# Performance work log

Hardware: AMD Instinct MI355X
Metric: run time of the kernel (lower is better)

## Reference

```python
import jax, jax.numpy as jnp
import numpy as np

VOCAB = 4096
CODE_DIM = 3
DECAY = 0.99
EPS = 1e-05


def setup_inputs() -> dict:
    key = jax.random.key(0)
    k1, k2, k3, k4 = jax.random.split(key, 4)
    feats = jax.random.normal(k1, (4, 8192, CODE_DIM), dtype=jnp.float32)
    embed = jax.random.normal(k2, (VOCAB, CODE_DIM), dtype=jnp.float32)
    ema_cluster_size = jax.random.uniform(k3, (VOCAB,), dtype=jnp.float32)
    ema_weight = jax.random.normal(k4, (VOCAB, CODE_DIM), dtype=jnp.float32)
    return {"feats": feats, "embed": embed,
            "ema_cluster_size": ema_cluster_size, "ema_weight": ema_weight}


def reference(feats, embed, ema_cluster_size, ema_weight):
    B, L, D = feats.shape
    flat = feats.reshape(-1, D)  # (N, D)
    # squared-euclidean distances to all codes: (N, V)
    dist = (jnp.sum(flat * flat, axis=1, keepdims=True)
            - 2.0 * flat @ embed.T
            + jnp.sum(embed * embed, axis=1))
    idx = jnp.argmin(dist, axis=1)  # (N,)
    quant = embed[idx].reshape(B, L, D)

    # EMA codebook update (training mode), done with segment_sum instead of a
    # dense (N, V) one-hot matmul -- same math.
    counts = jax.ops.segment_sum(jnp.ones_like(flat[:, 0]), idx, num_segments=VOCAB)
    sums = jax.ops.segment_sum(flat, idx, num_segments=VOCAB)  # (V, D)
    new_cluster_size = DECAY * ema_cluster_size + (1.0 - DECAY) * counts
    new_ema_weight = DECAY * ema_weight + (1.0 - DECAY) * sums
    n = jnp.sum(new_cluster_size)
    cluster_size = (new_cluster_size + EPS) / (n + VOCAB * EPS) * n
    new_embed = new_ema_weight / cluster_size[:, None]

    # VQ loss with stop-gradients matching torch detach semantics
    loss = (jnp.mean((quant - jax.lax.stop_gradient(feats)) ** 2)
            + 0.25 * jnp.mean((feats - jax.lax.stop_gradient(quant)) ** 2))
    # straight-through estimator
    quant_st = feats + jax.lax.stop_gradient(quant - feats)
    return (quant_st, idx.reshape(B, L), loss,
            new_cluster_size, new_ema_weight, new_embed)
```

## Files before the change

### kernel.cpp

```cpp
#include <hip/hip_runtime.h>
#include <math.h>

#pragma clang fp contract(off)

#define VOCAB 4096
#define NPTS  32768
#define NELEM 98304
#define BLOCK 256
#define NWAVE 4
#define CPW   (VOCAB / NWAVE)
#define PTS_PER_BLOCK 64

__global__ __launch_bounds__(BLOCK) void vq_assign(
    const float* __restrict__ feats, const float* __restrict__ embed,
    float* __restrict__ out_quant, float* __restrict__ out_idx,
    float* __restrict__ counts, float* __restrict__ sums,
    float* __restrict__ sse)
{
  extern __shared__ float smem[];
  float4* codes = (float4*)smem;
  float*  dbuf  = smem;
  int*    ibuf  = (int*)(smem + NWAVE * 64);

  const int tid  = threadIdx.x;
  const int lane = tid & 63;
  const int wv   = tid >> 6;

  for (int c = tid; c < VOCAB; c += BLOCK) {
    float e0 = embed[3 * c + 0];
    float e1 = embed[3 * c + 1];
    float e2 = embed[3 * c + 2];
    float esq = (e0 * e0 + e1 * e1) + e2 * e2;
    codes[c] = make_float4(e0, e1, e2, esq);
  }
  __syncthreads();

  const int p = blockIdx.x * PTS_PER_BLOCK + lane;
  const float x0 = feats[3 * p + 0];
  const float x1 = feats[3 * p + 1];
  const float x2 = feats[3 * p + 2];
  const float xsq = (x0 * x0 + x1 * x1) + x2 * x2;

  float best = INFINITY;
  int   bidx = 0;
  const float4* wc = codes + wv * CPW;
  const int cbase = wv * CPW;

  #pragma unroll 16
  for (int k = 0; k < CPW; ++k) {
    float4 e = wc[k];
    float dot = fmaf(x2, e.z, fmaf(x1, e.y, x0 * e.x));
    float d = (xsq - 2.0f * dot) + e.w;
    if (d < best) { best = d; bidx = cbase + k; }
  }

  __syncthreads();
  dbuf[wv * 64 + lane] = best;
  ibuf[wv * 64 + lane] = bidx;
  __syncthreads();

  if (wv == 0) {
    #pragma unroll
    for (int w = 1; w < NWAVE; ++w) {
      float od = dbuf[w * 64 + lane];
      int   oi = ibuf[w * 64 + lane];
      if (od < best || (od == best && oi < bidx)) { best = od; bidx = oi; }
    }

    const float q0 = embed[3 * bidx + 0];
    const float q1 = embed[3 * bidx + 1];
    const float q2 = embed[3 * bidx + 2];

    out_quant[3 * p + 0] = x0 + (q0 - x0);
    out_quant[3 * p + 1] = x1 + (q1 - x1);
    out_quant[3 * p + 2] = x2 + (q2 - x2);
    out_idx[p] = (float)bidx;

    atomicAdd(&counts[bidx], 1.0f);
    atomicAdd(&sums[3 * bidx + 0], x0);
    atomicAdd(&sums[3 * bidx + 1], x1);
    atomicAdd(&sums[3 * bidx + 2], x2);

    float d0 = q0 - x0, d1 = q1 - x1, d2 = q2 - x2;
    float l = (d0 * d0 + d1 * d1) + d2 * d2;
    #pragma unroll
    for (int m = 1; m <= 32; m <<= 1) l += __shfl_xor(l, m, 64);
    if (lane == 0) atomicAdd(sse, l);
  }
}

__global__ __launch_bounds__(1024) void vq_ema(
    const float* __restrict__ counts, const float* __restrict__ sums,
    const float* __restrict__ sse,
    const float* __restrict__ ema_cs, const float* __restrict__ ema_w,
    float* __restrict__ out_loss, float* __restrict__ out_ncs,
    float* __restrict__ out_nw, float* __restrict__ out_nemb)
{
  __shared__ float part[16];
  const int tid = threadIdx.x;
  const float DEC = 0.99f;
  const float OMD = (float)(1.0 - 0.99);
  const float EPS = 1e-5f;

  float ncs[4];
  float nw[12];
  float nsum = 0.0f;

  #pragma unroll
  for (int k = 0; k < 4; ++k) {
    int v = k * 1024 + tid;
    float t = DEC * ema_cs[v] + OMD * counts[v];
    ncs[k] = t;
    out_ncs[v] = t;
    nsum += t;
    #pragma unroll
    for (int d = 0; d < 3; ++d) {
      float w = DEC * ema_w[3 * v + d] + OMD * sums[3 * v + d];
      nw[3 * k + d] = w;
      out_nw[3 * v + d] = w;
    }
  }

  #pragma unroll
  for (int m = 1; m <= 32; m <<= 1) nsum += __shfl_xor(nsum, m, 64);
  if ((tid & 63) == 0) part[tid >> 6] = nsum;
  __syncthreads();

  float n = 0.0f;
  #pragma unroll
  for (int i = 0; i < 16; ++i) n += part[i];
  const float denom = n + (float)VOCAB * EPS;

  #pragma unroll
  for (int k = 0; k < 4; ++k) {
    int v = k * 1024 + tid;
    float cs = (ncs[k] + EPS) / denom * n;
    #pragma unroll
    for (int d = 0; d < 3; ++d)
      out_nemb[3 * v + d] = nw[3 * k + d] / cs;
  }

  if (tid == 0) {
    float m = sse[0] / (float)NELEM;
    out_loss[0] = m + 0.25f * m;
  }
}

extern "C" void kernel_launch(void* const* d_in, const int* in_sizes, int n_in,
                              void* d_out, int out_size, void* d_ws, size_t ws_size,
                              hipStream_t stream) {
  const float* feats  = (const float*)d_in[0];
  const float* embed  = (const float*)d_in[1];
  const float* ema_cs = (const float*)d_in[2];
  const float* ema_w  = (const float*)d_in[3];

  float* out      = (float*)d_out;
  float* o_quant  = out;
  float* o_idx    = out + 98304;
  float* o_loss   = out + 131072;
  float* o_ncs    = out + 131073;
  float* o_nw     = out + 135169;
  float* o_nemb   = out + 147457;

  float* ws_counts = (float*)d_ws;
  float* ws_sums   = ws_counts + VOCAB;
  float* ws_sse    = ws_sums + 3 * VOCAB;

  hipMemsetAsync(d_ws, 0, (size_t)(VOCAB * 4 + 1) * sizeof(float), stream);

  vq_assign<<<NPTS / PTS_PER_BLOCK, BLOCK, VOCAB * sizeof(float4), stream>>>(
      feats, embed, o_quant, o_idx, ws_counts, ws_sums, ws_sse);

  vq_ema<<<1, 1024, 0, stream>>>(
      ws_counts, ws_sums, ws_sse, ema_cs, ema_w,
      o_loss, o_ncs, o_nw, o_nemb);
}
```

Before: 52.10 us.

## Precompute packed codebook once and read it from global memory instead of LDS

Adds a small prep kernel that packs the codebook into float4 (xyz plus squared norm) in workspace once, instead of every one of the 512 blocks rebuilding the 64 KB table in shared memory. The assign kernel now streams codes straight from global memory with wave-uniform addresses, which the readfirstlane hint lets the compiler treat as scalar loads. This drops the per-block staging loop and one barrier, and frees LDS so more blocks can be resident. The cost is an extra kernel launch and reliance on cache or scalar-load bandwidth for the inner loop in place of LDS broadcast reads.

Result: slower. 92.33 us (+77.2%).

```diff
diff --git a/kernel.cpp b/kernel.cpp
--- a/kernel.cpp
+++ b/kernel.cpp
@@ -11,29 +11,29 @@
 #define CPW   (VOCAB / NWAVE)
 #define PTS_PER_BLOCK 64
 
+__global__ __launch_bounds__(256) void vq_prep(
+    const float* __restrict__ embed, float4* __restrict__ codes4)
+{
+  const int c = blockIdx.x * 256 + threadIdx.x;
+  float e0 = embed[3 * c + 0];
+  float e1 = embed[3 * c + 1];
+  float e2 = embed[3 * c + 2];
+  float esq = (e0 * e0 + e1 * e1) + e2 * e2;
+  codes4[c] = make_float4(e0, e1, e2, esq);
+}
+
 __global__ __launch_bounds__(BLOCK) void vq_assign(
-    const float* __restrict__ feats, const float* __restrict__ embed,
+    const float* __restrict__ feats, const float4* __restrict__ codes4,
     float* __restrict__ out_quant, float* __restrict__ out_idx,
     float* __restrict__ counts, float* __restrict__ sums,
     float* __restrict__ sse)
 {
-  extern __shared__ float smem[];
-  float4* codes = (float4*)smem;
-  float*  dbuf  = smem;
-  int*    ibuf  = (int*)(smem + NWAVE * 64);
+  __shared__ float dbuf[NWAVE][64];
+  __shared__ int   ibuf[NWAVE][64];
 
   const int tid  = threadIdx.x;
   const int lane = tid & 63;
-  const int wv   = tid >> 6;
-
-  for (int c = tid; c < VOCAB; c += BLOCK) {
-    float e0 = embed[3 * c + 0];
-    float e1 = embed[3 * c + 1];
-    float e2 = embed[3 * c + 2];
-    float esq = (e0 * e0 + e1 * e1) + e2 * e2;
-    codes[c] = make_float4(e0, e1, e2, esq);
-  }
-  __syncthreads();
+  const int wv   = __builtin_amdgcn_readfirstlane(tid >> 6);
 
   const int p = blockIdx.x * PTS_PER_BLOCK + lane;
   const float x0 = feats[3 * p + 0];
@@ -43,7 +43,7 @@
 
   float best = INFINITY;
   int   bidx = 0;
-  const float4* wc = codes + wv * CPW;
+  const float4* wc = codes4 + wv * CPW;
   const int cbase = wv * CPW;
 
   #pragma unroll 16
@@ -54,26 +54,23 @@
     if (d < best) { best = d; bidx = cbase + k; }
   }
 
-  __syncthreads();
-  dbuf[wv * 64 + lane] = best;
-  ibuf[wv * 64 + lane] = bidx;
+  dbuf[wv][lane] = best;
+  ibuf[wv][lane] = bidx;
   __syncthreads();
 
   if (wv == 0) {
     #pragma unroll
     for (int w = 1; w < NWAVE; ++w) {
-      float od = dbuf[w * 64 + lane];
-      int   oi = ibuf[w * 64 + lane];
+      float od = dbuf[w][lane];
+      int   oi = ibuf[w][lane];
       if (od < best || (od == best && oi < bidx)) { best = od; bidx = oi; }
     }
 
-    const float q0 = embed[3 * bidx + 0];
-    const float q1 = embed[3 * bidx + 1];
-    const float q2 = embed[3 * bidx + 2];
+    const float4 q = codes4[bidx];
 
-    out_quant[3 * p + 0] = x0 + (q0 - x0);
-    out_quant[3 * p + 1] = x1 + (q1 - x1);
-    out_quant[3 * p + 2] = x2 + (q2 - x2);
+    out_quant[3 * p + 0] = x0 + (q.x - x0);
+    out_quant[3 * p + 1] = x1 + (q.y - x1);
+    out_quant[3 * p + 2] = x2 + (q.z - x2);
     out_idx[p] = (float)bidx;
 
     atomicAdd(&counts[bidx], 1.0f);
@@ -81,7 +78,7 @@
     atomicAdd(&sums[3 * bidx + 1], x1);
     atomicAdd(&sums[3 * bidx + 2], x2);
 
-    float d0 = q0 - x0, d1 = q1 - x1, d2 = q2 - x2;
+    float d0 = q.x - x0, d1 = q.y - x1, d2 = q.z - x2;
     float l = (d0 * d0 + d1 * d1) + d2 * d2;
     #pragma unroll
     for (int m = 1; m <= 32; m <<= 1) l += __shfl_xor(l, m, 64);
@@ -165,11 +162,14 @@
   float* ws_counts = (float*)d_ws;
   float* ws_sums   = ws_counts + VOCAB;
   float* ws_sse    = ws_sums + 3 * VOCAB;
+  float4* ws_codes4 = (float4*)((float*)d_ws + 16400);
 
   hipMemsetAsync(d_ws, 0, (size_t)(VOCAB * 4 + 1) * sizeof(float), stream);
 
-  vq_assign<<<NPTS / PTS_PER_BLOCK, BLOCK, VOCAB * sizeof(float4), stream>>>(
-      feats, embed, o_quant, o_idx, ws_counts, ws_sums, ws_sse);
+  vq_prep<<<VOCAB / 256, 256, 0, stream>>>(embed, ws_codes4);
+
+  vq_assign<<<NPTS / PTS_PER_BLOCK, BLOCK, 0, stream>>>(
+      feats, ws_codes4, o_quant, o_idx, ws_counts, ws_sums, ws_sse);
 
   vq_ema<<<1, 1024, 0, stream>>>(
       ws_counts, ws_sums, ws_sse, ema_cs, ema_w,
```

## Process two points per lane and use eight waves per block

Applied to the files above, without the earlier changes.

Each lane now scores two points against every code, so each shared-memory codebook read is reused twice. The block grows to 512 threads with 8 waves, each sweeping a 512-code slice, and the grid halves to 256 blocks. The quantized vector is read from the shared codebook instead of global embed, and reduction buffers get their own static shared arrays, which removes the extra barrier. This raises register pressure per lane, and with only 256 blocks the GPU may be less well filled.

Result: no change. 51.68 us (-0.8%).

```diff
diff --git a/kernel.cpp b/kernel.cpp
--- a/kernel.cpp
+++ b/kernel.cpp
@@ -6,10 +6,11 @@
 #define VOCAB 4096
 #define NPTS  32768
 #define NELEM 98304
-#define BLOCK 256
-#define NWAVE 4
+#define BLOCK 512
+#define NWAVE 8
 #define CPW   (VOCAB / NWAVE)
-#define PTS_PER_BLOCK 64
+#define PPL   2
+#define PTS_PER_BLOCK (64 * PPL)
 
 __global__ __launch_bounds__(BLOCK) void vq_assign(
     const float* __restrict__ feats, const float* __restrict__ embed,
@@ -17,10 +18,9 @@
     float* __restrict__ counts, float* __restrict__ sums,
     float* __restrict__ sse)
 {
-  extern __shared__ float smem[];
-  float4* codes = (float4*)smem;
-  float*  dbuf  = smem;
-  int*    ibuf  = (int*)(smem + NWAVE * 64);
+  extern __shared__ float4 codes[];
+  __shared__ float dbuf[NWAVE][PPL][64];
+  __shared__ int   ibuf[NWAVE][PPL][64];
 
   const int tid  = threadIdx.x;
   const int lane = tid & 63;
@@ -35,57 +35,72 @@
   }
   __syncthreads();
 
-  const int p = blockIdx.x * PTS_PER_BLOCK + lane;
-  const float x0 = feats[3 * p + 0];
-  const float x1 = feats[3 * p + 1];
-  const float x2 = feats[3 * p + 2];
-  const float xsq = (x0 * x0 + x1 * x1) + x2 * x2;
+  const int pbase = blockIdx.x * PTS_PER_BLOCK;
+  float px[PPL][3], xsq[PPL];
+  #pragma unroll
+  for (int s = 0; s < PPL; ++s) {
+    const int p = pbase + s * 64 + lane;
+    px[s][0] = feats[3 * p + 0];
+    px[s][1] = feats[3 * p + 1];
+    px[s][2] = feats[3 * p + 2];
+    xsq[s] = (px[s][0] * px[s][0] + px[s][1] * px[s][1]) + px[s][2] * px[s][2];
+  }
 
-  float best = INFINITY;
-  int   bidx = 0;
+  float best[PPL] = {INFINITY, INFINITY};
+  int   bidx[PPL] = {0, 0};
   const float4* wc = codes + wv * CPW;
   const int cbase = wv * CPW;
 
   #pragma unroll 16
   for (int k = 0; k < CPW; ++k) {
     float4 e = wc[k];
-    float dot = fmaf(x2, e.z, fmaf(x1, e.y, x0 * e.x));
-    float d = (xsq - 2.0f * dot) + e.w;
-    if (d < best) { best = d; bidx = cbase + k; }
+    #pragma unroll
+    for (int s = 0; s < PPL; ++s) {
+      float dot = fmaf(px[s][2], e.z, fmaf(px[s][1], e.y, px[s][0] * e.x));
+      float d = (xsq[s] - 2.0f * dot) + e.w;
+      if (d < best[s]) { best[s] = d; bidx[s] = cbase + k; }
+    }
   }
 
-  __syncthreads();
-  dbuf[wv * 64 + lane] = best;
-  ibuf[wv * 64 + lane] = bidx;
+  #pragma unroll
+  for (int s = 0; s < PPL; ++s) {
+    dbuf[wv][s][lane] = best[s];
+    ibuf[wv][s][lane] = bidx[s];
+  }
   __syncthreads();
 
   if (wv == 0) {
     #pragma unroll
-    for (int w = 1; w < NWAVE; ++w) {
-      float od = dbuf[w * 64 + lane];
-      int   oi = ibuf[w * 64 + lane];
-      if (od < best || (od == best && oi < bidx)) { best = od; bidx = oi; }
+    for (int s = 0; s < PPL; ++s) {
+      float b = best[s];
+      int   bi = bidx[s];
+      #pragma unroll
+      for (int w = 1; w < NWAVE; ++w) {
+        float od = dbuf[w][s][lane];
+        int   oi = ibuf[w][s][lane];
+        if (od < b || (od == b && oi < bi)) { b = od; bi = oi; }
+      }
+
+      const int p = pbase + s * 64 + lane;
+      const float4 q = codes[bi];
+      const float x0 = px[s][0], x1 = px[s][1], x2 = px[s][2];
+
+      out_quant[3 * p + 0] = x0 + (q.x - x0);
+      out_quant[3 * p + 1] = x1 + (q.y - x1);
+      out_quant[3 * p + 2] = x2 + (q.z - x2);
+      out_idx[p] = (float)bi;
+
+      atomicAdd(&counts[bi], 1.0f);
+      atomicAdd(&sums[3 * bi + 0], x0);
+      atomicAdd(&sums[3 * bi + 1], x1);
+      atomicAdd(&sums[3 * bi + 2], x2);
+
+      float d0 = q.x - x0, d1 = q.y - x1, d2 = q.z - x2;
+      float l = (d0 * d0 + d1 * d1) + d2 * d2;
+      #pragma unroll
+      for (int m = 1; m <= 32; m <<= 1) l += __shfl_xor(l, m, 64);
+      if (lane == 0) atomicAdd(sse, l);
     }
-
-    const float q0 = embed[3 * bidx + 0];
-    const float q1 = embed[3 * bidx + 1];
-    const float q2 = embed[3 * bidx + 2];
-
-    out_quant[3 * p + 0] = x0 + (q0 - x0);
-    out_quant[3 * p + 1] = x1 + (q1 - x1);
-    out_quant[3 * p + 2] = x2 + (q2 - x2);
-    out_idx[p] = (float)bidx;
-
-    atomicAdd(&counts[bidx], 1.0f);
-    atomicAdd(&sums[3 * bidx + 0], x0);
-    atomicAdd(&sums[3 * bidx + 1], x1);
-    atomicAdd(&sums[3 * bidx + 2], x2);
-
-    float d0 = q0 - x0, d1 = q1 - x1, d2 = q2 - x2;
-    float l = (d0 * d0 + d1 * d1) + d2 * d2;
-    #pragma unroll
-    for (int m = 1; m <= 32; m <<= 1) l += __shfl_xor(l, m, 64);
-    if (lane == 0) atomicAdd(sse, l);
   }
 }
 
```

## Precompute codebook in prep kernel and split codes across 16-lane groups per point

Applied to the files above, without the earlier changes.

A new prep kernel zeroes the workspace, replacing the memset, and precomputes -2e and |e|^2 per code into a global float4 table. The assign kernel no longer stages the codebook in shared memory. Each 16-lane group handles 4 points, with each lane scanning a strided slice of codes using packed 2-wide FMAs. Per-lane argmins are merged with xor shuffles. This removes the 64KB LDS load per block and the cross-wave LDS reduction, and raises points per thread, at the cost of reading codes from global/L1 cache and a different FP rounding order for distances.

Result: slower. 63.61 us (+22.1%).

```diff
diff --git a/kernel.cpp b/kernel.cpp
--- a/kernel.cpp
+++ b/kernel.cpp
@@ -7,65 +7,118 @@
 #define NPTS  32768
 #define NELEM 98304
 #define BLOCK 256
-#define NWAVE 4
-#define CPW   (VOCAB / NWAVE)
-#define PTS_PER_BLOCK 64
-
-__global__ __launch_bounds__(BLOCK) void vq_assign(
+#define GRID  512
+
+typedef float v2f __attribute__((ext_vector_type(2)));
+
+static __device__ __forceinline__ v2f fma2(v2f a, v2f b, v2f c) {
+#if __has_builtin(__builtin_elementwise_fma)
+  return __builtin_elementwise_fma(a, b, c);
+#else
+  v2f r; r.x = fmaf(a.x, b.x, c.x); r.y = fmaf(a.y, b.y, c.y); return r;
+#endif
+}
+
+__global__ __launch_bounds__(256) void vq_prep(
+    const float* __restrict__ embed, float4* __restrict__ pc4,
+    float* __restrict__ wz)
+{
+  const int c = blockIdx.x * 256 + threadIdx.x;
+  #pragma unroll
+  for (int i = 0; i < 4; ++i) wz[4 * c + i] = 0.0f;
+  if (c == 0) wz[16384] = 0.0f;
+
+  float e0 = embed[3 * c + 0];
+  float e1 = embed[3 * c + 1];
+  float e2 = embed[3 * c + 2];
+  float esq = (e0 * e0 + e1 * e1) + e2 * e2;
+  pc4[c] = make_float4(-(e0 + e0), -(e1 + e1), -(e2 + e2), esq);
+}
+
+__global__ __launch_bounds__(BLOCK, 2) void vq_assign(
     const float* __restrict__ feats, const float* __restrict__ embed,
+    const float4* __restrict__ pc4,
     float* __restrict__ out_quant, float* __restrict__ out_idx,
     float* __restrict__ counts, float* __restrict__ sums,
     float* __restrict__ sse)
 {
-  extern __shared__ float smem[];
-  float4* codes = (float4*)smem;
-  float*  dbuf  = smem;
-  int*    ibuf  = (int*)(smem + NWAVE * 64);
-
   const int tid  = threadIdx.x;
   const int lane = tid & 63;
   const int wv   = tid >> 6;
-
-  for (int c = tid; c < VOCAB; c += BLOCK) {
-    float e0 = embed[3 * c + 0];
-    float e1 = embed[3 * c + 1];
-    float e2 = embed[3 * c + 2];
-    float esq = (e0 * e0 + e1 * e1) + e2 * e2;
-    codes[c] = make_float4(e0, e1, e2, esq);
-  }
-  __syncthreads();
-
-  const int p = blockIdx.x * PTS_PER_BLOCK + lane;
-  const float x0 = feats[3 * p + 0];
-  const float x1 = feats[3 * p + 1];
-  const float x2 = feats[3 * p + 2];
-  const float xsq = (x0 * x0 + x1 * x1) + x2 * x2;
-
-  float best = INFINITY;
-  int   bidx = 0;
-  const float4* wc = codes + wv * CPW;
-  const int cbase = wv * CPW;
-
-  #pragma unroll 16
-  for (int k = 0; k < CPW; ++k) {
-    float4 e = wc[k];
-    float dot = fmaf(x2, e.z, fmaf(x1, e.y, x0 * e.x));
-    float d = (xsq - 2.0f * dot) + e.w;
-    if (d < best) { best = d; bidx = cbase + k; }
-  }
-
-  __syncthreads();
-  dbuf[wv * 64 + lane] = best;
-  ibuf[wv * 64 + lane] = bidx;
-  __syncthreads();
-
-  if (wv == 0) {
-    #pragma unroll
-    for (int w = 1; w < NWAVE; ++w) {
-      float od = dbuf[w * 64 + lane];
-      int   oi = ibuf[w * 64 + lane];
-      if (od < best || (od == best && oi < bidx)) { best = od; bidx = oi; }
+  const int g    = lane >> 4;
+  const int gl   = lane & 15;
+  const int ggid = (blockIdx.x * 4 + wv) * 4 + g;
+  const int pbase = ggid * 4;
+
+  const float4* fp = (const float4*)(feats + 3 * pbase);
+  const float4 v0 = fp[0], v1 = fp[1], v2 = fp[2];
+
+  const float s0 = (v0.x * v0.x + v0.y * v0.y) + v0.z * v0.z;
+  const float s1 = (v0.w * v0.w + v1.x * v1.x) + v1.y * v1.y;
+  const float s2 = (v1.z * v1.z + v1.w * v1.w) + v2.x * v2.x;
+  const float s3 = (v2.y * v2.y + v2.z * v2.z) + v2.w * v2.w;
+
+  const v2f xa0 = {v0.x, v0.w}, xa1 = {v0.y, v1.x}, xa2 = {v0.z, v1.y};
+  const v2f xb0 = {v1.z, v2.y}, xb1 = {v1.w, v2.z}, xb2 = {v2.x, v2.w};
+  const v2f xqa = {s0, s1},     xqb = {s2, s3};
+
+  float bd0 = INFINITY, bd1 = INFINITY, bd2 = INFINITY, bd3 = INFINITY;
+  int   bk0 = 0, bk1 = 0, bk2 = 0, bk3 = 0;
+
+  const float4* cp = pc4 + gl;
+
+  #pragma unroll 8
+  for (int k = 0; k < VOCAB / 16; ++k) {
+    const float4 E = cp[16 * k];
+    const v2f e0 = {E.x, E.x}, e1 = {E.y, E.y}, e2 = {E.z, E.z};
+    const v2f es = {E.w, E.w};
+
+    v2f ta = xa0 * e0;
+    ta = fma2(xa1, e1, ta);
+    ta = fma2(xa2, e2, ta);
+    ta = ta + xqa;
+    ta = ta + es;
+
+    v2f tb = xb0 * e0;
+    tb = fma2(xb1, e1, tb);
+    tb = fma2(xb2, e2, tb);
+    tb = tb + xqb;
+    tb = tb + es;
+
+    if (ta.x < bd0) { bd0 = ta.x; bk0 = k; }
+    if (ta.y < bd1) { bd1 = ta.y; bk1 = k; }
+    if (tb.x < bd2) { bd2 = tb.x; bk2 = k; }
+    if (tb.y < bd3) { bd3 = tb.y; bk3 = k; }
+  }
+
+  float bd[4] = {bd0, bd1, bd2, bd3};
+  int   bi[4] = {16 * bk0 + gl, 16 * bk1 + gl, 16 * bk2 + gl, 16 * bk3 + gl};
+  #pragma unroll
+  for (int m = 1; m <= 8; m <<= 1) {
+    #pragma unroll
+    for (int j = 0; j < 4; ++j) {
+      float od = __shfl_xor(bd[j], m, 64);
+      int   oi = __shfl_xor(bi[j], m, 64);
+      if (od < bd[j] || (od == bd[j] && oi < bi[j])) { bd[j] = od; bi[j] = oi; }
     }
+  }
+
+  float l = 0.0f;
+  if (gl < 4) {
+    float b = bd[0];
+    int   bidx = bi[0];
+    float x0 = v0.x, x1 = v0.y, x2 = v0.z;
+    #pragma unroll
+    for (int j = 1; j < 4; ++j) {
+      if (gl == j) {
+        b = bd[j]; bidx = bi[j];
+        x0 = (j == 1) ? v0.w : ((j == 2) ? v1.z : v2.y);
+        x1 = (j == 1) ? v1.x : ((j == 2) ? v1.w : v2.z);
+        x2 = (j == 1) ? v1.y : ((j == 2) ? v2.x : v2.w);
+      }
+    }
+    (void)b;
+    const int p = pbase + gl;
 
     const float q0 = embed[3 * bidx + 0];
     const float q1 = embed[3 * bidx + 1];
@@ -82,11 +135,12 @@
     atomicAdd(&sums[3 * bidx + 2], x2);
 
     float d0 = q0 - x0, d1 = q1 - x1, d2 = q2 - x2;
-    float l = (d0 * d0 + d1 * d1) + d2 * d2;
-    #pragma unroll
-    for (int m = 1; m <= 32; m <<= 1) l += __shfl_xor(l, m, 64);
-    if (lane == 0) atomicAdd(sse, l);
-  }
+    l = (d0 * d0 + d1 * d1) + d2 * d2;
+  }
+
+  #pragma unroll
+  for (int m = 1; m <= 32; m <<= 1) l += __shfl_xor(l, m, 64);
+  if (lane == 0) atomicAdd(sse, l);
 }
 
 __global__ __launch_bounds__(1024) void vq_ema(
@@ -162,14 +216,16 @@
   float* o_nw     = out + 135169;
   float* o_nemb   = out + 147457;
 
-  float* ws_counts = (float*)d_ws;
-  float* ws_sums   = ws_counts + VOCAB;
-  float* ws_sse    = ws_sums + 3 * VOCAB;
-
-  hipMemsetAsync(d_ws, 0, (size_t)(VOCAB * 4 + 1) * sizeof(float), stream);
-
-  vq_assign<<<NPTS / PTS_PER_BLOCK, BLOCK, VOCAB * sizeof(float4), stream>>>(
-      feats, embed, o_quant, o_idx, ws_counts, ws_sums, ws_sse);
+  float*  ws_f      = (float*)d_ws;
+  float*  ws_counts = ws_f;
+  float*  ws_sums   = ws_f + 4096;
+  float*  ws_sse    = ws_f + 16384;
+  float4* ws_pc4    = (float4*)(ws_f + 16388);
+
+  vq_prep<<<VOCAB / 256, 256, 0, stream>>>(embed, ws_pc4, ws_f);
+
+  vq_assign<<<GRID, BLOCK, 0, stream>>>(
+      feats, embed, ws_pc4, o_quant, o_idx, ws_counts, ws_sums, ws_sse);
 
   vq_ema<<<1, 1024, 0, stream>>>(
       ws_counts, ws_sums, ws_sse, ema_cs, ema_w,
```
